# Kernel tuning notes

Hardware: AMD Instinct MI355X
Metric: run time of the kernel (lower is better)

Reference implementation:

```python
import jax, jax.numpy as jnp
import numpy as np

N, H, CIN, C, G = 50000, 16, 256, 256, 8
CPG = C // G          # 32 channels per group
CR = C // 4           # delta MLP hidden (delta_reduction=4)

def _lrelu(x):
    return jax.nn.leaky_relu(x, 0.1)

def setup_inputs() -> dict:
    key = jax.random.key(0)
    ks = jax.random.split(key, 16)
    def lin(k, fin, fout):
        return jax.random.normal(k, (fin, fout), jnp.float32) / np.sqrt(fin)
    return {
        'q_pts': jax.random.normal(ks[0], (N, 3), jnp.float32),
        's_pts': jax.random.normal(ks[1], (N, 3), jnp.float32),
        's_feats': jax.random.normal(ks[2], (N, CIN), jnp.float32),
        'neighb_inds': jax.random.randint(ks[3], (N, H), 0, N, jnp.int64),
        'Wq': lin(ks[4], CIN, C), 'bq': jnp.zeros((C,), jnp.float32),
        'Wk': lin(ks[5], CIN, C), 'bk': jnp.zeros((C,), jnp.float32),
        'Wv': lin(ks[6], CIN, C), 'bv': jnp.zeros((C,), jnp.float32),
        'Wd1': lin(ks[7], 3, CR), 'bd1': jnp.zeros((CR,), jnp.float32),
        'Wd2': lin(ks[8], CR, C), 'bd2': jnp.zeros((C,), jnp.float32),
        'Wa1': lin(ks[9], C, CPG), 'ba1': jnp.zeros((CPG,), jnp.float32),
        'Wa2': lin(ks[10], CPG, CPG), 'ba2': jnp.zeros((CPG,), jnp.float32),
    }

def reference(q_pts, s_pts, s_feats, neighb_inds,
              Wq, bq, Wk, bk, Wv, bv,
              Wd1, bd1, Wd2, bd2, Wa1, ba1, Wa2, ba2):
    # q/k/v projections  (N, C)
    v = s_feats @ Wv + bv
    k = s_feats @ Wk + bk
    q = s_feats @ Wq + bq
    # gather neighbor features (all indices < N, shadow mask is a no-op)
    nv = v[neighb_inds]                 # (N, H, C)
    nk = k[neighb_inds]                 # (N, H, C)
    # relative positions (torch.no_grad in source)
    rel = s_pts[neighb_inds] - q_pts[:, None, :]   # (N, H, 3)
    # delta MLP: 3 -> C/4 -> C (UnaryBlock + Linear, norm='none')
    geom = _lrelu(rel @ Wd1 + bd1) @ Wd2 + bd2     # (N, H, C)
    # geom_mode='sub': v-branch and qk-branch both subtract geom encodings
    nv = nv - geom
    # source always enters strided branch (s_pts padded before the check);
    # stride_mode='nearest' -> q feature of the first neighbor
    qf = q[neighb_inds[:, 0]]                      # (N, C)
    qk = qf[:, None, :] - nk - geom                # (N, H, C)
    # alpha MLP: NormBlock(id) + act, Linear C->CpG + act, Linear CpG->CpG
    a = _lrelu(qk)
    a = _lrelu(a @ Wa1 + ba1)
    a = a @ Wa2 + ba2                              # (N, H, CpG)
    attn = jax.nn.softmax(a, axis=1)               # softmax over neighbors
    # grouped weighted aggregation: C split as (CpG, G), attn broadcast over G
    out = (nv.reshape(N, H, CPG, G) * attn[..., None]).sum(axis=1)
    return out.reshape(N, C)
```

## Files before the change

kernel.cpp:

```cpp
#include <hip/hip_runtime.h>
#include <cstdint>
#include <cstddef>

#define N_PTS 50000
#define H 16
#define CIN 256
#define C 256
#define CPG 32
#define CR 64

typedef short bf16x8 __attribute__((ext_vector_type(8)));
typedef float f32x4 __attribute__((ext_vector_type(4)));

__device__ __forceinline__ unsigned short f2bf(float f) {
    unsigned int u = __float_as_uint(f);
    u += 0x7fff + ((u >> 16) & 1);
    return (unsigned short)(u >> 16);
}
__device__ __forceinline__ float bf2f(unsigned short s) {
    return __uint_as_float(((unsigned int)s) << 16);
}

__global__ __launch_bounds__(256) void convert_feats(
    const float* __restrict__ in, unsigned short* __restrict__ outp)
{
    size_t i = ((size_t)blockIdx.x * 256 + threadIdx.x) * 8;
    float4 f0 = *(const float4*)&in[i];
    float4 f1 = *(const float4*)&in[i + 4];
    unsigned short t[8] = {f2bf(f0.x), f2bf(f0.y), f2bf(f0.z), f2bf(f0.w),
                           f2bf(f1.x), f2bf(f1.y), f2bf(f1.z), f2bf(f1.w)};
    *(bf16x8*)&outp[i] = *(bf16x8*)t;
}

__global__ __launch_bounds__(256) void prep_frags(
    const float* __restrict__ Wd2, const float* __restrict__ Wa1,
    const float* __restrict__ Wa2, unsigned short* __restrict__ dst)
{
    int t = blockIdx.x * 256 + threadIdx.x;
    if (t >= 3200) return;
    const float* W; int Nc, NT, loc, base;
    if (t < 2048)      { W = Wd2; Nc = 256; NT = 16; loc = t;        base = 0; }
    else if (t < 3072) { W = Wa1; Nc = 32;  NT = 2;  loc = t - 2048; base = 16384; }
    else               { W = Wa2; Nc = 32;  NT = 2;  loc = t - 3072; base = 24576; }
    int f = loc >> 6, lane = loc & 63;
    int kt = f / NT, nt = f - kt * NT;
    int colc = nt * 16 + (lane & 15);
    int row0 = kt * 32 + ((lane >> 4) << 3);
    unsigned short tmp[8];
    #pragma unroll
    for (int j = 0; j < 8; ++j) tmp[j] = f2bf(W[(size_t)(row0 + j) * Nc + colc]);
    *(bf16x8*)&dst[(size_t)(base + loc * 8)] = *(bf16x8*)tmp;
}

__global__ __launch_bounds__(256) void prep_gemm_frags(
    const float* __restrict__ Wq, const float* __restrict__ Wk,
    const float* __restrict__ Wv, unsigned short* __restrict__ dst)
{
    int t = blockIdx.x * 256 + threadIdx.x;
    int lane = t & 63;
    int f = t >> 6;
    int ntg = f % 48;
    const float* W = ntg < 16 ? Wq : (ntg < 32 ? Wk : Wv);
    int colc = (ntg & 15) * 16 + (lane & 15);
    int row0 = (f / 48) * 32 + ((lane >> 4) << 3);
    unsigned short tmp[8];
    #pragma unroll
    for (int j = 0; j < 8; ++j) tmp[j] = f2bf(W[(size_t)(row0 + j) * 256 + colc]);
    *(bf16x8*)&dst[(size_t)t * 8] = *(bf16x8*)tmp;
}

__global__ __launch_bounds__(256) void qkv_gemm_mfma(
    const unsigned short* __restrict__ A,
    const unsigned short* __restrict__ wfrags,
    const float* __restrict__ bq, const float* __restrict__ bk,
    const float* __restrict__ bv, unsigned short* __restrict__ out)
{
    __shared__ unsigned short s_a[128 * 40];
    const int tid = threadIdx.x;
    const int lane = tid & 63, wave = tid >> 6;
    const int quad = lane >> 4, col16 = lane & 15;
    const int bx = blockIdx.x, by = blockIdx.y;

    f32x4 acc[2][8] = {};
    const int mrow = tid >> 1, half = tid & 1;
    const int gm = by * 128 + mrow;

    for (int kt = 0; kt < 8; ++kt) {
        bf16x8 a0 = {0,0,0,0,0,0,0,0}, a1 = a0;
        if (gm < N_PTS) {
            const unsigned short* src = &A[(size_t)gm * 256 + kt * 32 + half * 16];
            a0 = *(const bf16x8*)src;
            a1 = *(const bf16x8*)(src + 8);
        }
        __syncthreads();
        *(bf16x8*)&s_a[mrow * 40 + half * 16]     = a0;
        *(bf16x8*)&s_a[mrow * 40 + half * 16 + 8] = a1;
        __syncthreads();
        bf16x8 af0 = *(bf16x8*)&s_a[(wave * 32 + col16) * 40 + quad * 8];
        bf16x8 af1 = *(bf16x8*)&s_a[(wave * 32 + 16 + col16) * 40 + quad * 8];
        #pragma unroll
        for (int nt = 0; nt < 8; ++nt) {
            bf16x8 bf = *(const bf16x8*)&wfrags[(((size_t)kt * 48 + bx * 8 + nt) * 64 + lane) * 8];
            acc[0][nt] = __builtin_amdgcn_mfma_f32_16x16x32_bf16(af0, bf, acc[0][nt], 0, 0, 0);
            acc[1][nt] = __builtin_amdgcn_mfma_f32_16x16x32_bf16(af1, bf, acc[1][nt], 0, 0, 0);
        }
    }

    const int mode = bx >> 1;
    const float* bias = mode == 0 ? bq : (mode == 1 ? bk : bv);
    #pragma unroll
    for (int nt = 0; nt < 8; ++nt) {
        int cIn = (bx & 1) * 128 + nt * 16 + col16;
        float bb = bias[cIn];
        int pos = mode == 0 ? cIn : (256 + 2 * cIn + (mode == 2 ? 1 : 0));
        #pragma unroll
        for (int mt = 0; mt < 2; ++mt) {
            #pragma unroll
            for (int r = 0; r < 4; ++r) {
                int row = by * 128 + wave * 32 + mt * 16 + quad * 4 + r;
                if (row < N_PTS)
                    out[(size_t)row * 768 + pos] = f2bf(acc[mt][nt][r] + bb);
            }
        }
    }
}

#define D1S 72
#define GS 260
#define QKS 264
#define A1S 40
#define A2S 33

__global__ __launch_bounds__(256) void attn_mfma(
    const unsigned short* __restrict__ qkv,
    const float* __restrict__ q_pts, const float* __restrict__ s_pts,
    const int* __restrict__ nbr,
    const float* __restrict__ Wd1, const float* __restrict__ bd1,
    const float* __restrict__ bd2,
    const unsigned short* __restrict__ frags,
    const float* __restrict__ ba1, const float* __restrict__ ba2,
    float* __restrict__ out)
{
    __shared__ unsigned short s_d1[H * D1S];
    __shared__ float          s_geom[H * GS];
    __shared__ unsigned short s_qk[H * QKS];
    __shared__ unsigned short s_a1[H * A1S];
    __shared__ float          s_a2[H * A2S];
    __shared__ float          s_rel[4][H][3];
    __shared__ int            s_idx[4][H];

    const int tid = threadIdx.x;
    const int lane = tid & 63, wave = tid >> 6;
    const int quad = lane >> 4, col = lane & 15;
    const int n0 = blockIdx.x * 4;
    const int c = tid;

    if (tid < 64) {
        int pp = tid >> 4, hh = tid & 15;
        int idx = nbr[(size_t)(n0 + pp) * H + hh];
        s_idx[pp][hh] = idx;
        #pragma unroll
        for (int x = 0; x < 3; ++x)
            s_rel[pp][hh][x] = s_pts[(size_t)idx * 3 + x] - q_pts[(size_t)(n0 + pp) * 3 + x];
    }

    const float w1x = Wd1[lane], w1y = Wd1[64 + lane], w1z = Wd1[128 + lane];
    const float b1 = bd1[lane];
    const float b2 = bd2[c];
    bf16x8 wd2f[2][4];
    #pragma unroll
    for (int t = 0; t < 4; ++t) {
        wd2f[0][t] = *(const bf16x8*)&frags[((size_t)((0 * 16 + wave * 4 + t) * 64 + lane)) * 8];
        wd2f[1][t] = *(const bf16x8*)&frags[((size_t)((1 * 16 + wave * 4 + t) * 64 + lane)) * 8];
    }
    bf16x8 wa1f[8];
    bf16x8 wa2f = {0,0,0,0,0,0,0,0};
    if (wave < 2) {
        #pragma unroll
        for (int kt = 0; kt < 8; ++kt)
            wa1f[kt] = *(const bf16x8*)&frags[16384 + ((size_t)((kt * 2 + wave) * 64 + lane)) * 8];
        wa2f = *(const bf16x8*)&frags[24576 + ((size_t)(wave * 64 + lane)) * 8];
    }
    __syncthreads();

    for (int p = 0; p < 4; ++p) {
        const int n = n0 + p;

        #pragma unroll
        for (int pass = 0; pass < 4; ++pass) {
            int h = pass * 4 + wave;
            float v = b1 + s_rel[p][h][0] * w1x + s_rel[p][h][1] * w1y + s_rel[p][h][2] * w1z;
            s_d1[h * D1S + lane] = f2bf(fmaxf(v, 0.1f * v));
        }
        __syncthreads();

        {
            bf16x8 ga = *(bf16x8*)&s_d1[col * D1S + quad * 8];
            bf16x8 gb = *(bf16x8*)&s_d1[col * D1S + 32 + quad * 8];
            #pragma unroll
            for (int t = 0; t < 4; ++t) {
                f32x4 acc = {0.f, 0.f, 0.f, 0.f};
                acc = __builtin_amdgcn_mfma_f32_16x16x32_bf16(ga, wd2f[0][t], acc, 0, 0, 0);
                acc = __builtin_amdgcn_mfma_f32_16x16x32_bf16(gb, wd2f[1][t], acc, 0, 0, 0);
                int nt = wave * 4 + t;
                #pragma unroll
                for (int rr = 0; rr < 4; ++rr)
                    s_geom[(quad * 4 + rr) * GS + nt * 16 + col] = acc[rr];
            }
        }
        __syncthreads();

        float qf = bf2f(qkv[(size_t)s_idx[p][0] * 768 + c]);
        float vg[H];
        #pragma unroll
        for (int h = 0; h < H; ++h) {
            int idx = s_idx[p][h];
            unsigned int u = *(const unsigned int*)&qkv[(size_t)idx * 768 + 256 + 2 * c];
            float nk = __uint_as_float(u << 16);
            float nv = __uint_as_float(u & 0xffff0000u);
            float g = s_geom[h * GS + c] + b2;
            vg[h] = nv - g;
            float tq = qf - nk - g;
            s_qk[h * QKS + c] = f2bf(fmaxf(tq, 0.1f * tq));
        }
        __syncthreads();

        if (wave < 2) {
            f32x4 acc = {0.f, 0.f, 0.f, 0.f};
            #pragma unroll
            for (int kt = 0; kt < 8; ++kt) {
                bf16x8 a = *(bf16x8*)&s_qk[col * QKS + kt * 32 + quad * 8];
                acc = __builtin_amdgcn_mfma_f32_16x16x32_bf16(a, wa1f[kt], acc, 0, 0, 0);
            }
            int j = wave * 16 + col;
            float bb = ba1[j];
            #pragma unroll
            for (int rr = 0; rr < 4; ++rr) {
                float v = acc[rr] + bb;
                s_a1[(quad * 4 + rr) * A1S + j] = f2bf(fmaxf(v, 0.1f * v));
            }
        }
        __syncthreads();

        if (wave < 2) {
            bf16x8 aa = *(bf16x8*)&s_a1[col * A1S + quad * 8];
            f32x4 acc = {0.f, 0.f, 0.f, 0.f};
            acc = __builtin_amdgcn_mfma_f32_16x16x32_bf16(aa, wa2f, acc, 0, 0, 0);
            int j = wave * 16 + col;
            float bb = ba2[j];
            #pragma unroll
            for (int rr = 0; rr < 4; ++rr)
                s_a2[(quad * 4 + rr) * A2S + j] = acc[rr] + bb;
        }
        __syncthreads();

        if (wave == 0) {
            int j = lane & 31, hb = (lane >> 5) * 8;
            float vals[8];
            float mx = -1e30f;
            #pragma unroll
            for (int i = 0; i < 8; ++i) {
                vals[i] = s_a2[(hb + i) * A2S + j];
                mx = fmaxf(mx, vals[i]);
            }
            mx = fmaxf(mx, __shfl_xor(mx, 32));
            float sum = 0.f;
            #pragma unroll
            for (int i = 0; i < 8; ++i) { vals[i] = __expf(vals[i] - mx); sum += vals[i]; }
            sum += __shfl_xor(sum, 32);
            float inv = 1.f / sum;
            #pragma unroll
            for (int i = 0; i < 8; ++i) s_a2[(hb + i) * A2S + j] = vals[i] * inv;
        }
        __syncthreads();

        float o = 0.f;
        const int aj = c >> 3;
        #pragma unroll
        for (int h = 0; h < H; ++h) o += vg[h] * s_a2[h * A2S + aj];
        out[(size_t)n * C + c] = o;
    }
}


extern "C" void kernel_launch(void* const* d_in, const int* in_sizes, int n_in,
                              void* d_out, int out_size, void* d_ws, size_t ws_size,
                              hipStream_t stream) {
    const float* q_pts   = (const float*)d_in[0];
    const float* s_pts   = (const float*)d_in[1];
    const float* s_feats = (const float*)d_in[2];
    const int*   nbr     = (const int*)d_in[3];
    const float* Wq  = (const float*)d_in[4];
    const float* bq  = (const float*)d_in[5];
    const float* Wk  = (const float*)d_in[6];
    const float* bk  = (const float*)d_in[7];
    const float* Wv  = (const float*)d_in[8];
    const float* bv  = (const float*)d_in[9];
    const float* Wd1 = (const float*)d_in[10];
    const float* bd1 = (const float*)d_in[11];
    const float* Wd2 = (const float*)d_in[12];
    const float* bd2 = (const float*)d_in[13];
    const float* Wa1 = (const float*)d_in[14];
    const float* ba1 = (const float*)d_in[15];
    const float* Wa2 = (const float*)d_in[16];
    const float* ba2 = (const float*)d_in[17];

    float* out = (float*)d_out;
    char* ws = (char*)d_ws;
    unsigned short* A_bf16    = (unsigned short*)(ws);
    unsigned short* qkvb      = (unsigned short*)(ws + 25600000);
    unsigned short* attnFrags = (unsigned short*)(ws + 102400000);
    unsigned short* gemmFrags = (unsigned short*)(ws + 102451200);

    convert_feats<<<6250, 256, 0, stream>>>(s_feats, A_bf16);
    prep_frags<<<13, 256, 0, stream>>>(Wd2, Wa1, Wa2, attnFrags);
    prep_gemm_frags<<<96, 256, 0, stream>>>(Wq, Wk, Wv, gemmFrags);

    dim3 g1(6, (N_PTS + 127) / 128);
    qkv_gemm_mfma<<<g1, 256, 0, stream>>>(A_bf16, gemmFrags, bq, bk, bv, qkvb);

    attn_mfma<<<(N_PTS / 4), 256, 0, stream>>>(qkvb, q_pts, s_pts, nbr,
                                               Wd1, bd1, bd2, attnFrags,
                                               ba1, ba2, out);
}
```

Before: 426.9 us.

## Merge prep kernels, stage full A tile via async LDS loads, store geom as bf16

Merges three preprocessing kernels into one launch. The QKV GEMM now loads the whole 128x256 bf16 A tile into LDS up front with global_load_lds and an XOR swizzle, replacing eight sync-heavy K-step loads. The GEMM then keeps all A fragments in registers. The attention kernel stores the geometry encoding in LDS as bf16 rather than fp32, halving that buffer. Costs are 64KB of LDS per GEMM block, which lowers occupancy, higher register pressure, and less precision in geom.

```diff
diff --git a/kernel.cpp b/kernel.cpp
--- a/kernel.cpp
+++ b/kernel.cpp
@@ -20,53 +20,58 @@
 __device__ __forceinline__ float bf2f(unsigned short s) {
     return __uint_as_float(((unsigned int)s) << 16);
 }
-
-__global__ __launch_bounds__(256) void convert_feats(
-    const float* __restrict__ in, unsigned short* __restrict__ outp)
+__device__ __forceinline__ void async_load16(const void* g, void* l) {
+    __builtin_amdgcn_global_load_lds(
+        (const __attribute__((address_space(1))) unsigned int*)g,
+        (__attribute__((address_space(3))) unsigned int*)l, 16, 0, 0);
+}
+
+__global__ __launch_bounds__(256) void prep_all(
+    const float* __restrict__ feats,
+    const float* __restrict__ Wq, const float* __restrict__ Wk,
+    const float* __restrict__ Wv,
+    const float* __restrict__ Wd2, const float* __restrict__ Wa1,
+    const float* __restrict__ Wa2,
+    unsigned short* __restrict__ A_bf16,
+    unsigned short* __restrict__ gemmFrags,
+    unsigned short* __restrict__ attnFrags)
 {
-    size_t i = ((size_t)blockIdx.x * 256 + threadIdx.x) * 8;
-    float4 f0 = *(const float4*)&in[i];
-    float4 f1 = *(const float4*)&in[i + 4];
-    unsigned short t[8] = {f2bf(f0.x), f2bf(f0.y), f2bf(f0.z), f2bf(f0.w),
-                           f2bf(f1.x), f2bf(f1.y), f2bf(f1.z), f2bf(f1.w)};
-    *(bf16x8*)&outp[i] = *(bf16x8*)t;
-}
-
-__global__ __launch_bounds__(256) void prep_frags(
-    const float* __restrict__ Wd2, const float* __restrict__ Wa1,
-    const float* __restrict__ Wa2, unsigned short* __restrict__ dst)
-{
-    int t = blockIdx.x * 256 + threadIdx.x;
-    if (t >= 3200) return;
-    const float* W; int Nc, NT, loc, base;
-    if (t < 2048)      { W = Wd2; Nc = 256; NT = 16; loc = t;        base = 0; }
-    else if (t < 3072) { W = Wa1; Nc = 32;  NT = 2;  loc = t - 2048; base = 16384; }
-    else               { W = Wa2; Nc = 32;  NT = 2;  loc = t - 3072; base = 24576; }
-    int f = loc >> 6, lane = loc & 63;
-    int kt = f / NT, nt = f - kt * NT;
-    int colc = nt * 16 + (lane & 15);
-    int row0 = kt * 32 + ((lane >> 4) << 3);
-    unsigned short tmp[8];
-    #pragma unroll
-    for (int j = 0; j < 8; ++j) tmp[j] = f2bf(W[(size_t)(row0 + j) * Nc + colc]);
-    *(bf16x8*)&dst[(size_t)(base + loc * 8)] = *(bf16x8*)tmp;
-}
-
-__global__ __launch_bounds__(256) void prep_gemm_frags(
-    const float* __restrict__ Wq, const float* __restrict__ Wk,
-    const float* __restrict__ Wv, unsigned short* __restrict__ dst)
-{
-    int t = blockIdx.x * 256 + threadIdx.x;
-    int lane = t & 63;
-    int f = t >> 6;
-    int ntg = f % 48;
-    const float* W = ntg < 16 ? Wq : (ntg < 32 ? Wk : Wv);
-    int colc = (ntg & 15) * 16 + (lane & 15);
-    int row0 = (f / 48) * 32 + ((lane >> 4) << 3);
-    unsigned short tmp[8];
-    #pragma unroll
-    for (int j = 0; j < 8; ++j) tmp[j] = f2bf(W[(size_t)(row0 + j) * 256 + colc]);
-    *(bf16x8*)&dst[(size_t)t * 8] = *(bf16x8*)tmp;
+    int bid = blockIdx.x;
+    if (bid < 6250) {
+        size_t i = ((size_t)bid * 256 + threadIdx.x) * 8;
+        float4 f0 = *(const float4*)&feats[i];
+        float4 f1 = *(const float4*)&feats[i + 4];
+        unsigned short t[8] = {f2bf(f0.x), f2bf(f0.y), f2bf(f0.z), f2bf(f0.w),
+                               f2bf(f1.x), f2bf(f1.y), f2bf(f1.z), f2bf(f1.w)};
+        *(bf16x8*)&A_bf16[i] = *(bf16x8*)t;
+    } else if (bid < 6346) {
+        int t = (bid - 6250) * 256 + threadIdx.x;
+        int lane = t & 63;
+        int f = t >> 6;
+        int ntg = f % 48;
+        const float* W = ntg < 16 ? Wq : (ntg < 32 ? Wk : Wv);
+        int colc = (ntg & 15) * 16 + (lane & 15);
+        int row0 = (f / 48) * 32 + ((lane >> 4) << 3);
+        unsigned short tmp[8];
+        #pragma unroll
+        for (int j = 0; j < 8; ++j) tmp[j] = f2bf(W[(size_t)(row0 + j) * 256 + colc]);
+        *(bf16x8*)&gemmFrags[(size_t)t * 8] = *(bf16x8*)tmp;
+    } else {
+        int t = (bid - 6346) * 256 + threadIdx.x;
+        if (t >= 3200) return;
+        const float* W; int Nc, NT, loc, base;
+        if (t < 2048)      { W = Wd2; Nc = 256; NT = 16; loc = t;        base = 0; }
+        else if (t < 3072) { W = Wa1; Nc = 32;  NT = 2;  loc = t - 2048; base = 16384; }
+        else               { W = Wa2; Nc = 32;  NT = 2;  loc = t - 3072; base = 24576; }
+        int f = loc >> 6, lane = loc & 63;
+        int kt = f / NT, nt = f - kt * NT;
+        int colc = nt * 16 + (lane & 15);
+        int row0 = kt * 32 + ((lane >> 4) << 3);
+        unsigned short tmp[8];
+        #pragma unroll
+        for (int j = 0; j < 8; ++j) tmp[j] = f2bf(W[(size_t)(row0 + j) * Nc + colc]);
+        *(bf16x8*)&attnFrags[(size_t)(base + loc * 8)] = *(bf16x8*)tmp;
+    }
 }
 
 __global__ __launch_bounds__(256) void qkv_gemm_mfma(
@@ -75,34 +80,46 @@
     const float* __restrict__ bq, const float* __restrict__ bk,
     const float* __restrict__ bv, unsigned short* __restrict__ out)
 {
-    __shared__ unsigned short s_a[128 * 40];
+    __shared__ unsigned short s_a[128 * 256];
     const int tid = threadIdx.x;
     const int lane = tid & 63, wave = tid >> 6;
     const int quad = lane >> 4, col16 = lane & 15;
     const int bx = blockIdx.x, by = blockIdx.y;
+    const int row0 = by * 128;
+
+    #pragma unroll
+    for (int t = 0; t < 16; ++t) {
+        int base = (wave * 16 + t) * 512;
+        int o = base + lane * 8;
+        int row = o >> 8;
+        int cb = (o >> 3) & 31;
+        int cbo = cb ^ ((row & 7) << 2);
+        int gr = row0 + row;
+        if (gr >= N_PTS) gr = N_PTS - 1;
+        async_load16(A + (size_t)gr * 256 + cbo * 8, s_a + base);
+    }
+    __syncthreads();
+
+    bf16x8 af[2][8];
+    #pragma unroll
+    for (int mt = 0; mt < 2; ++mt) {
+        int row = wave * 32 + mt * 16 + col16;
+        int rsw = (row & 7) << 5;
+        #pragma unroll
+        for (int kt = 0; kt < 8; ++kt) {
+            int uo = (kt * 32 + quad * 8) ^ rsw;
+            af[mt][kt] = *(const bf16x8*)&s_a[row * 256 + uo];
+        }
+    }
 
     f32x4 acc[2][8] = {};
-    const int mrow = tid >> 1, half = tid & 1;
-    const int gm = by * 128 + mrow;
-
+    #pragma unroll
     for (int kt = 0; kt < 8; ++kt) {
-        bf16x8 a0 = {0,0,0,0,0,0,0,0}, a1 = a0;
-        if (gm < N_PTS) {
-            const unsigned short* src = &A[(size_t)gm * 256 + kt * 32 + half * 16];
-            a0 = *(const bf16x8*)src;
-            a1 = *(const bf16x8*)(src + 8);
-        }
-        __syncthreads();
-        *(bf16x8*)&s_a[mrow * 40 + half * 16]     = a0;
-        *(bf16x8*)&s_a[mrow * 40 + half * 16 + 8] = a1;
-        __syncthreads();
-        bf16x8 af0 = *(bf16x8*)&s_a[(wave * 32 + col16) * 40 + quad * 8];
-        bf16x8 af1 = *(bf16x8*)&s_a[(wave * 32 + 16 + col16) * 40 + quad * 8];
         #pragma unroll
         for (int nt = 0; nt < 8; ++nt) {
             bf16x8 bf = *(const bf16x8*)&wfrags[(((size_t)kt * 48 + bx * 8 + nt) * 64 + lane) * 8];
-            acc[0][nt] = __builtin_amdgcn_mfma_f32_16x16x32_bf16(af0, bf, acc[0][nt], 0, 0, 0);
-            acc[1][nt] = __builtin_amdgcn_mfma_f32_16x16x32_bf16(af1, bf, acc[1][nt], 0, 0, 0);
+            acc[0][nt] = __builtin_amdgcn_mfma_f32_16x16x32_bf16(af[0][kt], bf, acc[0][nt], 0, 0, 0);
+            acc[1][nt] = __builtin_amdgcn_mfma_f32_16x16x32_bf16(af[1][kt], bf, acc[1][nt], 0, 0, 0);
         }
     }
 
@@ -117,7 +134,7 @@
         for (int mt = 0; mt < 2; ++mt) {
             #pragma unroll
             for (int r = 0; r < 4; ++r) {
-                int row = by * 128 + wave * 32 + mt * 16 + quad * 4 + r;
+                int row = row0 + wave * 32 + mt * 16 + quad * 4 + r;
                 if (row < N_PTS)
                     out[(size_t)row * 768 + pos] = f2bf(acc[mt][nt][r] + bb);
             }
@@ -126,7 +143,7 @@
 }
 
 #define D1S 72
-#define GS 260
+#define GSB 268
 #define QKS 264
 #define A1S 40
 #define A2S 33
@@ -142,7 +159,7 @@
     float* __restrict__ out)
 {
     __shared__ unsigned short s_d1[H * D1S];
-    __shared__ float          s_geom[H * GS];
+    __shared__ unsigned short s_geom[H * GSB];
     __shared__ unsigned short s_qk[H * QKS];
     __shared__ unsigned short s_a1[H * A1S];
     __shared__ float          s_a2[H * A2S];
@@ -205,7 +222,7 @@
                 int nt = wave * 4 + t;
                 #pragma unroll
                 for (int rr = 0; rr < 4; ++rr)
-                    s_geom[(quad * 4 + rr) * GS + nt * 16 + col] = acc[rr];
+                    s_geom[(quad * 4 + rr) * GSB + nt * 16 + col] = f2bf(acc[rr]);
             }
         }
         __syncthreads();
@@ -218,7 +235,7 @@
             unsigned int u = *(const unsigned int*)&qkv[(size_t)idx * 768 + 256 + 2 * c];
             float nk = __uint_as_float(u << 16);
             float nv = __uint_as_float(u & 0xffff0000u);
-            float g = s_geom[h * GS + c] + b2;
+            float g = bf2f(s_geom[h * GSB + c]) + b2;
             vg[h] = nv - g;
             float tq = qf - nk - g;
             s_qk[h * QKS + c] = f2bf(fmaxf(tq, 0.1f * tq));
@@ -312,9 +329,8 @@
     unsigned short* attnFrags = (unsigned short*)(ws + 102400000);
     unsigned short* gemmFrags = (unsigned short*)(ws + 102451200);
 
-    convert_feats<<<6250, 256, 0, stream>>>(s_feats, A_bf16);
-    prep_frags<<<13, 256, 0, stream>>>(Wd2, Wa1, Wa2, attnFrags);
-    prep_gemm_frags<<<96, 256, 0, stream>>>(Wq, Wk, Wv, gemmFrags);
+    prep_all<<<6359, 256, 0, stream>>>(s_feats, Wq, Wk, Wv, Wd2, Wa1, Wa2,
+                                       A_bf16, gemmFrags, attnFrags);
 
     dim3 g1(6, (N_PTS + 127) / 128);
     qkv_gemm_mfma<<<g1, 256, 0, stream>>>(A_bf16, gemmFrags, bq, bk, bv, qkvb);
```

After: 458.4 us. 7.4% more time.
